# Optimization experiments

Hardware: AMD Instinct MI355X
Metric: run time of the kernel (lower is better)

## Reference

```python
import jax, jax.numpy as jnp
import numpy as np

INF = 1e10  # stand-in for +inf boundary of soft-DTW DP (safe under exp(-INF/gamma)=0)
HUBER_DELTA = 1.0
SDTW_ALPHA = 0.1
SDTW_GAMMA = 0.1


def _softmin3(a, b, c, gamma):
    # soft-min_gamma(a,b,c) = -gamma * logsumexp(-a/g, -b/g, -c/g)
    s = jnp.stack([a, b, c], axis=0) * (-1.0 / gamma)
    return -gamma * jax.nn.logsumexp(s, axis=0)


def _soft_dtw(x, y, gamma):
    # x, y: (B, L, C). Returns per-batch soft-DTW value R[L-1, L-1], shape (B,).
    B, L, C = x.shape
    # pairwise squared-euclidean distances (B, L, L) without (B,L,L,C) blowup
    x2 = jnp.sum(x * x, axis=-1)  # (B, L)
    y2 = jnp.sum(y * y, axis=-1)  # (B, L)
    D = x2[:, :, None] + y2[:, None, :] - 2.0 * jnp.einsum('blc,bmc->blm', x, y)

    i = jnp.arange(L)

    # Diagonals are stored as (B, L+1) arrays indexed by p = i + 1, so that the
    # virtual cell R[-1,-1] = 0 lives at p = 0 of diagonal k = -2.
    def step(carry, k):
        r2, r1 = carry  # diagonals k-2 and k-1
        j = k - i
        valid = (j >= 0) & (j < L)
        jc = jnp.clip(j, 0, L - 1)
        d = jnp.take_along_axis(D, jc[None, :, None], axis=2)[:, :, 0]  # (B, L) = D[:, i, k-i]
        a = r2[:, :-1]  # R[i-1, j-1]
        b = r1[:, :-1]  # R[i-1, j]
        c = r1[:, 1:]   # R[i, j-1]
        rk_vals = jnp.where(valid[None, :], d + _softmin3(a, b, c, gamma), INF)
        rk = jnp.concatenate([jnp.full((B, 1), INF, D.dtype), rk_vals], axis=1)
        return (r1, rk), None

    r2 = jnp.full((B, L + 1), INF, D.dtype).at[:, 0].set(0.0)  # diag k=-2: R[-1,-1]=0
    r1 = jnp.full((B, L + 1), INF, D.dtype)                    # diag k=-1: all inf
    (_, rlast), _ = jax.lax.scan(step, (r2, r1), jnp.arange(2 * L - 1))
    return rlast[:, L]  # R[L-1, L-1] per batch


def _huber_mean(x_hat, x, delta):
    d = x_hat - x
    ad = jnp.abs(d)
    loss = jnp.where(ad <= delta, 0.5 * d * d, delta * (ad - 0.5 * delta))
    return jnp.mean(loss)


def setup_inputs() -> dict:
    key = jax.random.key(0)
    k1, k2, k3 = jax.random.split(key, 3)
    B, L, C = 64, 512, 16
    x = jax.random.normal(k1, (B, L, C), dtype=jnp.float32)
    x_hat = jax.random.normal(k2, (B, L, C), dtype=jnp.float32)
    commitment_loss = jax.random.uniform(k3, (), dtype=jnp.float32)
    return {"x": x, "x_hat": x_hat, "commitment_loss": commitment_loss}


def reference(x, x_hat, commitment_loss):
    huber = _huber_mean(x_hat, x, HUBER_DELTA)
    sdtw = jnp.mean(_soft_dtw(x, x_hat, SDTW_GAMMA)) * SDTW_ALPHA
    total = huber + sdtw + commitment_loss
    # stacked [total, huber, sdtw, commitment] (torch module returns a dict of these scalars)
    return jnp.stack([total, huber, sdtw, commitment_loss])
```

## Files before the change

kernel.cpp:

```cpp
#include <hip/hip_runtime.h>
#include <math.h>


#define INFV 1.0e10f
static constexpr float kC1 = 14.4269504088896f;
static constexpr float kC2 = 0.0693147180559945f;

__device__ __forceinline__ int diag_off(int k) {
  if (k <= 512) return (k * (k + 1)) >> 1;
  int u = k - 512;
  return 131328 + 511 * u - ((u * (u - 1)) >> 1);
}
__device__ __forceinline__ int diag_i0(int k) { return k < 512 ? 0 : k - 511; }

__device__ __forceinline__ float huber1(float d) {
  float ad = fabsf(d);
  return ad <= 1.0f ? 0.5f * d * d : ad - 0.5f;
}

__global__ __launch_bounds__(256) void huber_kernel(const float* __restrict__ x,
                                                    const float* __restrict__ xh,
                                                    float* __restrict__ part) {
  int t = threadIdx.x;
  int gid = blockIdx.x * 256 + t;
  float s = 0.f;
  for (int i = gid; i < 131072; i += 65536) {
    float4 a = ((const float4*)x)[i];
    float4 b = ((const float4*)xh)[i];
    s += huber1(b.x - a.x) + huber1(b.y - a.y) + huber1(b.z - a.z) + huber1(b.w - a.w);
  }
  for (int o = 32; o > 0; o >>= 1) s += __shfl_down(s, o, 64);
  __shared__ float ws4[4];
  if ((t & 63) == 0) ws4[t >> 6] = s;
  __syncthreads();
  if (t == 0) part[blockIdx.x] = ws4[0] + ws4[1] + ws4[2] + ws4[3];
}

__global__ __launch_bounds__(256) void gemm_diag_kernel(const float* __restrict__ x,
                                                        const float* __restrict__ xh,
                                                        float* __restrict__ Dp) {
  const int b = blockIdx.z;
  const int ti = blockIdx.x;
  const int tj = blockIdx.y;
  const int t = threadIdx.x;
  __shared__ float sm[64 * 67];
  float* xsT = sm;
  float* ysT = sm + 16 * 68;
  const float* xb = x + ((size_t)b * 8192) + ti * 1024;
  const float* yb = xh + ((size_t)b * 8192) + tj * 1024;
  {
    float4 xv = ((const float4*)xb)[t];
    float4 yv = ((const float4*)yb)[t];
    int r = t >> 2, c0 = (t & 3) << 2;
    xsT[(c0 + 0) * 68 + r] = xv.x;
    xsT[(c0 + 1) * 68 + r] = xv.y;
    xsT[(c0 + 2) * 68 + r] = xv.z;
    xsT[(c0 + 3) * 68 + r] = xv.w;
    ysT[(c0 + 0) * 68 + r] = yv.x;
    ysT[(c0 + 1) * 68 + r] = yv.y;
    ysT[(c0 + 2) * 68 + r] = yv.z;
    ysT[(c0 + 3) * 68 + r] = yv.w;
  }
  __syncthreads();
  const int tm = t & 15, tn = t >> 4;
  float acc[4][4] = {};
  float y2a[4] = {};
#pragma unroll
  for (int c = 0; c < 16; ++c) {
    float4 xv = *(const float4*)&xsT[c * 68 + tm * 4];
    float4 yv = *(const float4*)&ysT[c * 68 + tn * 4];
    float xr[4] = {xv.x, xv.y, xv.z, xv.w};
    float yr[4] = {yv.x, yv.y, yv.z, yv.w};
#pragma unroll
    for (int n = 0; n < 4; ++n) {
      y2a[n] = fmaf(yr[n], yr[n], y2a[n]);
#pragma unroll
      for (int m = 0; m < 4; ++m) acc[m][n] = fmaf(xr[m], yr[n], acc[m][n]);
    }
  }
  __syncthreads();
#pragma unroll
  for (int m = 0; m < 4; ++m)
#pragma unroll
    for (int n = 0; n < 4; ++n)
      sm[(tm * 4 + m) * 67 + (tn * 4 + n)] = acc[m][n] - 0.5f * y2a[n];
  __syncthreads();
  const int lane = t & 63, wv = t >> 6;
  float* outb = Dp + (size_t)b * 262144;
  const int kbase = ti * 64 + tj * 64;
  for (int s = wv; s < 127; s += 4) {
    int ilo = s > 63 ? s - 63 : 0;
    int ihi = s < 63 ? s : 63;
    if (lane >= ilo && lane <= ihi) {
      float v = sm[lane * 67 + (s - lane)];
      int k = kbase + s;
      outb[diag_off(k) - diag_i0(k) + (ti * 64 + lane)] = v;
    }
  }
}

#define DTW_STEP(PD, W, R1, R2)                                             \
  do {                                                                      \
    int j = k - tid;                                                        \
    bool valid = (j >= 0) && (j < 512);                                     \
    float av = R2[tid];                                                     \
    float bv = R1[tid];                                                     \
    float dotv = PD;                                                        \
    if (k + 3 <= 1022) PD = Db[diag_off(k + 3) - diag_i0(k + 3) + tid];     \
    float mv = fminf(fminf(av, bv), vprev);                                 \
    float ssum = exp2f((mv - av) * kC1) + exp2f((mv - bv) * kC1) +          \
                 exp2f((mv - vprev) * kC1);                                 \
    float sm3 = fmaf(-kC2, log2f(ssum), mv);                                \
    float dd = fmaf(-2.0f, dotv, x2);                                       \
    float val = valid ? (dd + sm3) : INFV;                                  \
    W[tid + 1] = val;                                                       \
    vprev = val;                                                            \
    __syncthreads();                                                        \
    ++k;                                                                    \
  } while (0)

__global__ __launch_bounds__(512) void dtw_kernel(const float* __restrict__ x,
                                                  const float* __restrict__ Dp,
                                                  float* __restrict__ outv) {
  const int b = blockIdx.x;
  const int tid = threadIdx.x;
  __shared__ float rA[516], rB[516], rC[516];
  const float* xr = x + (size_t)b * 8192 + tid * 16;
  float x2 = 0.f;
#pragma unroll
  for (int c = 0; c < 16; c += 4) {
    float4 v = *(const float4*)(xr + c);
    x2 += v.x * v.x + v.y * v.y + v.z * v.z + v.w * v.w;
  }
  rA[tid] = INFV;
  rB[tid] = INFV;
  rC[tid] = INFV;
  if (tid == 0) { rA[512] = INFV; rB[512] = INFV; rC[512] = INFV; }
  const float* Db = Dp + (size_t)b * 262144;
  float p0 = Db[tid];
  float p1 = Db[1 + tid];
  float p2 = Db[3 + tid];
  float d00 = fmaf(-2.0f, p0, x2);
  float vprev = (tid == 0) ? d00 : INFV;
  if (tid == 0) rC[1] = d00;
  p0 = Db[diag_off(3) + tid];
  int k = 1;
  __syncthreads();
#pragma unroll 1
  for (int it = 0; it < 340; ++it) {
    DTW_STEP(p1, rA, rC, rB);
    DTW_STEP(p2, rB, rA, rC);
    DTW_STEP(p0, rC, rB, rA);
  }
  DTW_STEP(p1, rA, rC, rB);
  DTW_STEP(p2, rB, rA, rC);
  if (tid == 511) outv[b] = vprev;
}

__device__ __forceinline__ float dot16(const float4& a, const float4& b2,
                                       const float4& c, const float4& d,
                                       const float4* yp) {
  float4 q0 = yp[0], q1 = yp[1], q2 = yp[2], q3 = yp[3];
  float s = a.x * q0.x;
  s = fmaf(a.y, q0.y, s); s = fmaf(a.z, q0.z, s); s = fmaf(a.w, q0.w, s);
  s = fmaf(b2.x, q1.x, s); s = fmaf(b2.y, q1.y, s); s = fmaf(b2.z, q1.z, s); s = fmaf(b2.w, q1.w, s);
  s = fmaf(c.x, q2.x, s); s = fmaf(c.y, q2.y, s); s = fmaf(c.z, q2.z, s); s = fmaf(c.w, q2.w, s);
  s = fmaf(d.x, q3.x, s); s = fmaf(d.y, q3.y, s); s = fmaf(d.z, q3.z, s); s = fmaf(d.w, q3.w, s);
  return s;
}

#define DTW_FSTEP(W, R1, R2)                                                \
  do {                                                                      \
    int j = k - tid;                                                        \
    bool valid = (j >= 0) && (j < 512);                                     \
    int jc = valid ? j : 0;                                                 \
    float av = R2[tid];                                                     \
    float bv = R1[tid];                                                     \
    float dotv = dot16(xa, xb4, xc4, xd4, (const float4*)&ysl[jc * 20]);    \
    float mv = fminf(fminf(av, bv), vprev);                                 \
    float ssum = exp2f((mv - av) * kC1) + exp2f((mv - bv) * kC1) +          \
                 exp2f((mv - vprev) * kC1);                                 \
    float sm3 = fmaf(-kC2, log2f(ssum), mv);                                \
    float dd = fmaf(-2.0f, dotv, x2 + y2s[jc]);                             \
    float val = valid ? (dd + sm3) : INFV;                                  \
    W[tid + 1] = val;                                                       \
    vprev = val;                                                            \
    __syncthreads();                                                        \
    ++k;                                                                    \
  } while (0)

__global__ __launch_bounds__(512) void dtw_fused_kernel(const float* __restrict__ x,
                                                        const float* __restrict__ xh,
                                                        float* __restrict__ outv) {
  const int b = blockIdx.x;
  const int tid = threadIdx.x;
  __shared__ float ysl[512 * 20];
  __shared__ float y2s[512];
  __shared__ float rA[516], rB[516], rC[516];
  const float* xr = x + (size_t)b * 8192 + tid * 16;
  const float* yr = xh + (size_t)b * 8192 + tid * 16;
  float4 xa = *(const float4*)(xr + 0);
  float4 xb4 = *(const float4*)(xr + 4);
  float4 xc4 = *(const float4*)(xr + 8);
  float4 xd4 = *(const float4*)(xr + 12);
  float x2 = xa.x * xa.x + xa.y * xa.y + xa.z * xa.z + xa.w * xa.w +
             xb4.x * xb4.x + xb4.y * xb4.y + xb4.z * xb4.z + xb4.w * xb4.w +
             xc4.x * xc4.x + xc4.y * xc4.y + xc4.z * xc4.z + xc4.w * xc4.w +
             xd4.x * xd4.x + xd4.y * xd4.y + xd4.z * xd4.z + xd4.w * xd4.w;
  {
    float4 q0 = *(const float4*)(yr + 0);
    float4 q1 = *(const float4*)(yr + 4);
    float4 q2 = *(const float4*)(yr + 8);
    float4 q3 = *(const float4*)(yr + 12);
    *(float4*)&ysl[tid * 20 + 0] = q0;
    *(float4*)&ysl[tid * 20 + 4] = q1;
    *(float4*)&ysl[tid * 20 + 8] = q2;
    *(float4*)&ysl[tid * 20 + 12] = q3;
    y2s[tid] = q0.x * q0.x + q0.y * q0.y + q0.z * q0.z + q0.w * q0.w +
               q1.x * q1.x + q1.y * q1.y + q1.z * q1.z + q1.w * q1.w +
               q2.x * q2.x + q2.y * q2.y + q2.z * q2.z + q2.w * q2.w +
               q3.x * q3.x + q3.y * q3.y + q3.z * q3.z + q3.w * q3.w;
  }
  rA[tid] = INFV;
  rB[tid] = INFV;
  rC[tid] = INFV;
  if (tid == 0) { rA[512] = INFV; rB[512] = INFV; rC[512] = INFV; }
  __syncthreads();
  float dot00 = dot16(xa, xb4, xc4, xd4, (const float4*)&ysl[0]);
  float d00 = fmaf(-2.0f, dot00, x2 + y2s[0]);
  float vprev = (tid == 0) ? d00 : INFV;
  if (tid == 0) rC[1] = d00;
  int k = 1;
  __syncthreads();
#pragma unroll 1
  for (int it = 0; it < 340; ++it) {
    DTW_FSTEP(rA, rC, rB);
    DTW_FSTEP(rB, rA, rC);
    DTW_FSTEP(rC, rB, rA);
  }
  DTW_FSTEP(rA, rC, rB);
  DTW_FSTEP(rB, rA, rC);
  if (tid == 511) outv[b] = vprev;
}

__global__ __launch_bounds__(256) void finalize_kernel(const float* __restrict__ part,
                                                       const float* __restrict__ dtwv,
                                                       const float* __restrict__ commit,
                                                       float* __restrict__ out) {
  int t = threadIdx.x;
  float h = part[t];
  float dv = (t < 64) ? dtwv[t] : 0.f;
  for (int o = 32; o > 0; o >>= 1) {
    h += __shfl_down(h, o, 64);
    dv += __shfl_down(dv, o, 64);
  }
  __shared__ float sh[4], sd[4];
  if ((t & 63) == 0) { sh[t >> 6] = h; sd[t >> 6] = dv; }
  __syncthreads();
  if (t == 0) {
    float hs = sh[0] + sh[1] + sh[2] + sh[3];
    float ds = sd[0] + sd[1] + sd[2] + sd[3];
    float hm = hs * (1.0f / 524288.0f);
    float smv = ds * (0.1f / 64.0f);
    float cm = commit[0];
    out[0] = hm + smv + cm;
    out[1] = hm;
    out[2] = smv;
    out[3] = cm;
  }
}

extern "C" void kernel_launch(void* const* d_in, const int* in_sizes, int n_in,
                              void* d_out, int out_size, void* d_ws, size_t ws_size,
                              hipStream_t stream) {
  (void)in_sizes; (void)n_in; (void)out_size;
  const float* x = (const float*)d_in[0];
  const float* xh = (const float*)d_in[1];
  const float* commit = (const float*)d_in[2];
  float* out = (float*)d_out;
  float* ws = (float*)d_ws;
  float* part = ws;
  float* dtwv = ws + 256;
  float* Dp = ws + 512;
  const size_t need = 2048 + (size_t)64 * 262144 * 4;

  huber_kernel<<<256, 256, 0, stream>>>(x, xh, part);
  if (ws_size >= need) {
    gemm_diag_kernel<<<dim3(8, 8, 64), 256, 0, stream>>>(x, xh, Dp);
    dtw_kernel<<<64, 512, 0, stream>>>(x, Dp, dtwv);
  } else {
    dtw_fused_kernel<<<64, 512, 0, stream>>>(x, xh, dtwv);
  }
  finalize_kernel<<<1, 256, 0, stream>>>(part, dtwv, commit, out);
}
```

Baseline: 383.9 us.

## Replace per-diagonal block barriers with wavefront-pipelined soft-DTW using shuffles and flags

Replaces the original DTW kernel, which called __syncthreads after every anti-diagonal step. In the new kernel each 64-lane wavefront owns 64 rows and passes the neighbouring cell by __shfl_up within the wave. Between waves, the last lane's values go through a shared-memory ring buffer guarded by spin-wait flags, checked once every 10 steps. Softmin now sorts its three inputs with min/med3/max, which saves one exp2 per cell. D loads are prefetched 10 diagonals ahead. Spin-waiting on volatile shared flags adds pipeline fill latency and depends on memory ordering being correct.

```diff
diff --git a/kernel.cpp b/kernel.cpp
--- a/kernel.cpp
+++ b/kernel.cpp
@@ -99,61 +99,84 @@
   }
 }
 
-#define DTW_STEP(PD, W, R1, R2)                                             \
+#define PSTEP(PN)                                                           \
   do {                                                                      \
-    int j = k - tid;                                                        \
-    bool valid = (j >= 0) && (j < 512);                                     \
-    float av = R2[tid];                                                     \
-    float bv = R1[tid];                                                     \
-    float dotv = PD;                                                        \
-    if (k + 3 <= 1022) PD = Db[diag_off(k + 3) - diag_i0(k + 3) + tid];     \
-    float mv = fminf(fminf(av, bv), vprev);                                 \
-    float ssum = exp2f((mv - av) * kC1) + exp2f((mv - bv) * kC1) +          \
-                 exp2f((mv - vprev) * kC1);                                 \
+    float bval = __shfl_up(vprev, 1);                                       \
+    float rv = ringPrev[min(kk + 63, 574)];                                 \
+    if (lane == 0) bval = (w == 0) ? INFV : rv;                             \
+    float mv = fminf(fminf(aval, bval), vprev);                             \
+    float md = __builtin_amdgcn_fmed3f(aval, bval, vprev);                  \
+    float mx = fmaxf(fmaxf(aval, bval), vprev);                             \
+    float ssum = 1.0f + exp2f((mv - md) * kC1) + exp2f((mv - mx) * kC1);    \
     float sm3 = fmaf(-kC2, log2f(ssum), mv);                                \
+    float dotv = PN;                                                        \
+    {                                                                       \
+      int kc = k0 + min(kk + 10, 574);                                      \
+      PN = DbL[diag_off(kc) - diag_i0(kc)];                                 \
+    }                                                                       \
     float dd = fmaf(-2.0f, dotv, x2);                                       \
-    float val = valid ? (dd + sm3) : INFV;                                  \
-    W[tid + 1] = val;                                                       \
+    float val = ((unsigned)(kk - lane) <= 511u) ? (dd + sm3) : INFV;        \
+    if (lane == 63) ringOwn[kk] = val;                                      \
+    aval = bval;                                                            \
     vprev = val;                                                            \
-    __syncthreads();                                                        \
-    ++k;                                                                    \
+    ++kk;                                                                   \
   } while (0)
 
-__global__ __launch_bounds__(512) void dtw_kernel(const float* __restrict__ x,
-                                                  const float* __restrict__ Dp,
-                                                  float* __restrict__ outv) {
+__global__ __launch_bounds__(512) void dtw_pipe_kernel(const float* __restrict__ x,
+                                                       const float* __restrict__ Dp,
+                                                       float* __restrict__ outv) {
   const int b = blockIdx.x;
   const int tid = threadIdx.x;
-  __shared__ float rA[516], rB[516], rC[516];
-  const float* xr = x + (size_t)b * 8192 + tid * 16;
+  const int w = tid >> 6;
+  const int lane = tid & 63;
+  __shared__ float ring[8][576];
+  __shared__ int flags[8];
+  if (tid < 8) flags[tid] = 0;
+  __syncthreads();
+  volatile int* vflags = flags;
+
+  const int i = (w << 6) | lane;
+  const float* xr = x + (size_t)b * 8192 + i * 16;
   float x2 = 0.f;
 #pragma unroll
   for (int c = 0; c < 16; c += 4) {
     float4 v = *(const float4*)(xr + c);
     x2 += v.x * v.x + v.y * v.y + v.z * v.z + v.w * v.w;
   }
-  rA[tid] = INFV;
-  rB[tid] = INFV;
-  rC[tid] = INFV;
-  if (tid == 0) { rA[512] = INFV; rB[512] = INFV; rC[512] = INFV; }
-  const float* Db = Dp + (size_t)b * 262144;
-  float p0 = Db[tid];
-  float p1 = Db[1 + tid];
-  float p2 = Db[3 + tid];
-  float d00 = fmaf(-2.0f, p0, x2);
-  float vprev = (tid == 0) ? d00 : INFV;
-  if (tid == 0) rC[1] = d00;
-  p0 = Db[diag_off(3) + tid];
-  int k = 1;
-  __syncthreads();
+  const float* DbL = Dp + (size_t)b * 262144 + i;
+  const int k0 = w << 6;
+
+  float p[10];
+#pragma unroll
+  for (int n = 0; n < 10; ++n) {
+    int kg = k0 + n;
+    p[n] = DbL[diag_off(kg) - diag_i0(kg)];
+  }
+
+  float aval = (w == 0 && lane == 0) ? 0.0f : INFV;
+  float vprev = INFV;
+  float* ringOwn = ring[w];
+  const float* ringPrev = ring[(w == 0) ? 7 : (w - 1)];
+
+  int kk = 0;
 #pragma unroll 1
-  for (int it = 0; it < 340; ++it) {
-    DTW_STEP(p1, rA, rC, rB);
-    DTW_STEP(p2, rB, rA, rC);
-    DTW_STEP(p0, rC, rB, rA);
-  }
-  DTW_STEP(p1, rA, rC, rB);
-  DTW_STEP(p2, rB, rA, rC);
+  for (int ss = 0; ss < 58; ++ss) {
+    const int nsub = (ss == 57) ? 5 : 10;
+    if (w != 0) {
+      const int need = min(kk + nsub + 63, 575);
+      while (vflags[w - 1] < need) {
+      }
+      __threadfence_block();
+    }
+    if (nsub == 10) {
+      PSTEP(p[0]); PSTEP(p[1]); PSTEP(p[2]); PSTEP(p[3]); PSTEP(p[4]);
+      PSTEP(p[5]); PSTEP(p[6]); PSTEP(p[7]); PSTEP(p[8]); PSTEP(p[9]);
+    } else {
+      PSTEP(p[0]); PSTEP(p[1]); PSTEP(p[2]); PSTEP(p[3]); PSTEP(p[4]);
+    }
+    __threadfence_block();
+    if (lane == 63) vflags[w] = kk;
+  }
   if (tid == 511) outv[b] = vprev;
 }
 
@@ -164,7 +187,7 @@
   float s = a.x * q0.x;
   s = fmaf(a.y, q0.y, s); s = fmaf(a.z, q0.z, s); s = fmaf(a.w, q0.w, s);
   s = fmaf(b2.x, q1.x, s); s = fmaf(b2.y, q1.y, s); s = fmaf(b2.z, q1.z, s); s = fmaf(b2.w, q1.w, s);
-  s = fmaf(c.x, q2.x, s); s = fmaf(c.y, q2.y, s); s = fmaf(c.z, q2.z, s); s = fmaf(c.w, q2.w, s);
+  s = fmaf(c.x, q2.x, s); s = fmaf(c.y, q2.y, s); s = fmaf(c.w, q2.w, s); s = fmaf(c.z, q2.z, s);
   s = fmaf(d.x, q3.x, s); s = fmaf(d.y, q3.y, s); s = fmaf(d.z, q3.z, s); s = fmaf(d.w, q3.w, s);
   return s;
 }
@@ -287,7 +310,7 @@
   huber_kernel<<<256, 256, 0, stream>>>(x, xh, part);
   if (ws_size >= need) {
     gemm_diag_kernel<<<dim3(8, 8, 64), 256, 0, stream>>>(x, xh, Dp);
-    dtw_kernel<<<64, 512, 0, stream>>>(x, Dp, dtwv);
+    dtw_pipe_kernel<<<64, 512, 0, stream>>>(x, Dp, dtwv);
   } else {
     dtw_fused_kernel<<<64, 512, 0, stream>>>(x, xh, dtwv);
   }
```

After: 353.0 us. 8.1% less time.

## Run soft-DTW wavefront in one wave with 8 rows per lane via DPP

Applied to the files above, without the earlier changes.

Replaces the 512-thread, LDS-plus-barrier-per-diagonal DTW with a single 64-lane wavefront where each lane owns 8 consecutive rows in registers. Neighbour values move between lanes through DPP row shifts instead of shared memory and __syncthreads. The GEMM now writes a full pre-scaled (by 1/(gamma·ln2)) distance matrix transposed in row-major j order, replacing the diagonal-packed layout. The softmin is rewritten as min plus log2(1+2^(min-med)+2^(min-max)) with fmed3. This removes about 1000 block-wide barriers but serialises 8 cells per lane per step, and wave-level cross-row shifting must handle the row-of-16 boundaries correctly.

```diff
diff --git a/kernel.cpp b/kernel.cpp
--- a/kernel.cpp
+++ b/kernel.cpp
@@ -2,16 +2,9 @@
 #include <math.h>
 
 
-#define INFV 1.0e10f
+#define INFS 1.0e10f
 static constexpr float kC1 = 14.4269504088896f;
 static constexpr float kC2 = 0.0693147180559945f;
-
-__device__ __forceinline__ int diag_off(int k) {
-  if (k <= 512) return (k * (k + 1)) >> 1;
-  int u = k - 512;
-  return 131328 + 511 * u - ((u * (u - 1)) >> 1);
-}
-__device__ __forceinline__ int diag_i0(int k) { return k < 512 ? 0 : k - 511; }
 
 __device__ __forceinline__ float huber1(float d) {
   float ad = fabsf(d);
@@ -38,14 +31,13 @@
 
 __global__ __launch_bounds__(256) void gemm_diag_kernel(const float* __restrict__ x,
                                                         const float* __restrict__ xh,
-                                                        float* __restrict__ Dp) {
+                                                        float* __restrict__ E) {
   const int b = blockIdx.z;
   const int ti = blockIdx.x;
   const int tj = blockIdx.y;
   const int t = threadIdx.x;
-  __shared__ float sm[64 * 67];
-  float* xsT = sm;
-  float* ysT = sm + 16 * 68;
+  __shared__ float xsT[16 * 68];
+  __shared__ float ysT[16 * 68];
   const float* xb = x + ((size_t)b * 8192) + ti * 1024;
   const float* yb = xh + ((size_t)b * 8192) + tj * 1024;
   {
@@ -65,6 +57,7 @@
   const int tm = t & 15, tn = t >> 4;
   float acc[4][4] = {};
   float y2a[4] = {};
+  float x2a[4] = {};
 #pragma unroll
   for (int c = 0; c < 16; ++c) {
     float4 xv = *(const float4*)&xsT[c * 68 + tm * 4];
@@ -77,84 +70,94 @@
 #pragma unroll
       for (int m = 0; m < 4; ++m) acc[m][n] = fmaf(xr[m], yr[n], acc[m][n]);
     }
-  }
-  __syncthreads();
-#pragma unroll
-  for (int m = 0; m < 4; ++m)
-#pragma unroll
-    for (int n = 0; n < 4; ++n)
-      sm[(tm * 4 + m) * 67 + (tn * 4 + n)] = acc[m][n] - 0.5f * y2a[n];
-  __syncthreads();
-  const int lane = t & 63, wv = t >> 6;
-  float* outb = Dp + (size_t)b * 262144;
-  const int kbase = ti * 64 + tj * 64;
-  for (int s = wv; s < 127; s += 4) {
-    int ilo = s > 63 ? s - 63 : 0;
-    int ihi = s < 63 ? s : 63;
-    if (lane >= ilo && lane <= ihi) {
-      float v = sm[lane * 67 + (s - lane)];
-      int k = kbase + s;
-      outb[diag_off(k) - diag_i0(k) + (ti * 64 + lane)] = v;
-    }
-  }
-}
-
-#define DTW_STEP(PD, W, R1, R2)                                             \
-  do {                                                                      \
-    int j = k - tid;                                                        \
-    bool valid = (j >= 0) && (j < 512);                                     \
-    float av = R2[tid];                                                     \
-    float bv = R1[tid];                                                     \
-    float dotv = PD;                                                        \
-    if (k + 3 <= 1022) PD = Db[diag_off(k + 3) - diag_i0(k + 3) + tid];     \
-    float mv = fminf(fminf(av, bv), vprev);                                 \
-    float ssum = exp2f((mv - av) * kC1) + exp2f((mv - bv) * kC1) +          \
-                 exp2f((mv - vprev) * kC1);                                 \
-    float sm3 = fmaf(-kC2, log2f(ssum), mv);                                \
-    float dd = fmaf(-2.0f, dotv, x2);                                       \
-    float val = valid ? (dd + sm3) : INFV;                                  \
-    W[tid + 1] = val;                                                       \
-    vprev = val;                                                            \
-    __syncthreads();                                                        \
-    ++k;                                                                    \
+#pragma unroll
+    for (int m = 0; m < 4; ++m) x2a[m] = fmaf(xr[m], xr[m], x2a[m]);
+  }
+  float* Eb = E + (size_t)b * 262144;
+  const int icol = ti * 64 + tm * 4;
+#pragma unroll
+  for (int n = 0; n < 4; ++n) {
+    int jrow = tj * 64 + tn * 4 + n;
+    float4 o;
+    o.x = kC1 * fmaf(-2.0f, acc[0][n], x2a[0] + y2a[n]);
+    o.y = kC1 * fmaf(-2.0f, acc[1][n], x2a[1] + y2a[n]);
+    o.z = kC1 * fmaf(-2.0f, acc[2][n], x2a[2] + y2a[n]);
+    o.w = kC1 * fmaf(-2.0f, acc[3][n], x2a[3] + y2a[n]);
+    *(float4*)&Eb[(size_t)jrow * 512 + icol] = o;
+  }
+}
+
+__device__ __forceinline__ float cellv(float a, float b, float c, float d) {
+  float mv = fminf(fminf(a, b), c);
+  float md = __builtin_amdgcn_fmed3f(a, b, c);
+  float mx = fmaxf(fmaxf(a, b), c);
+  float e1 = exp2f(mv - md);
+  float e2 = exp2f(mv - mx);
+  float lg = log2f(1.0f + e1 + e2);
+  return mv + d - lg;
+}
+
+#define STEP(P)                                                                        \
+  do {                                                                                 \
+    float r7old = R7;                                                                  \
+    int vi7 = __float_as_int(r7old);                                                   \
+    float bs = __int_as_float(__builtin_amdgcn_update_dpp(0, vi7, 0x111, 0xF, 0xF, true)); \
+    float bbr = __int_as_float(__builtin_amdgcn_update_dpp(0, vi7, 0x142, 0xF, 0xF, true)); \
+    float tb = fixl ? bbr : bs;                                                        \
+    tb = isl0 ? INFS : tb;                                                             \
+    float old0 = R0; R0 = cellv(taPrev, tb, R0, eL##P.x);                              \
+    float old1 = R1; R1 = cellv(old0, R0, R1, eL##P.y);                                \
+    float old2 = R2; R2 = cellv(old1, R1, R2, eL##P.z);                                \
+    float old3 = R3; R3 = cellv(old2, R2, R3, eL##P.w);                                \
+    float old4 = R4; R4 = cellv(old3, R3, R4, eH##P.x);                                \
+    float old5 = R5; R5 = cellv(old4, R4, R5, eH##P.y);                                \
+    float old6 = R6; R6 = cellv(old5, R5, R6, eH##P.z);                                \
+    R7 = cellv(old6, R6, R7, eH##P.w);                                                 \
+    taPrev = tb;                                                                       \
+    int jn = s + 4 - t;                                                                \
+    jn = jn < 0 ? 0 : (jn > 511 ? 511 : jn);                                           \
+    const float4* ep = (const float4*)(baseL + ((size_t)jn << 9));                     \
+    eL##P = ep[0];                                                                     \
+    eH##P = ep[1];                                                                     \
+    ++s;                                                                               \
   } while (0)
 
-__global__ __launch_bounds__(512) void dtw_kernel(const float* __restrict__ x,
-                                                  const float* __restrict__ Dp,
-                                                  float* __restrict__ outv) {
+__global__ __launch_bounds__(64) void dtw_r8_kernel(const float* __restrict__ E,
+                                                    float* __restrict__ outv) {
   const int b = blockIdx.x;
-  const int tid = threadIdx.x;
-  __shared__ float rA[516], rB[516], rC[516];
-  const float* xr = x + (size_t)b * 8192 + tid * 16;
-  float x2 = 0.f;
-#pragma unroll
-  for (int c = 0; c < 16; c += 4) {
-    float4 v = *(const float4*)(xr + c);
-    x2 += v.x * v.x + v.y * v.y + v.z * v.z + v.w * v.w;
-  }
-  rA[tid] = INFV;
-  rB[tid] = INFV;
-  rC[tid] = INFV;
-  if (tid == 0) { rA[512] = INFV; rB[512] = INFV; rC[512] = INFV; }
-  const float* Db = Dp + (size_t)b * 262144;
-  float p0 = Db[tid];
-  float p1 = Db[1 + tid];
-  float p2 = Db[3 + tid];
-  float d00 = fmaf(-2.0f, p0, x2);
-  float vprev = (tid == 0) ? d00 : INFV;
-  if (tid == 0) rC[1] = d00;
-  p0 = Db[diag_off(3) + tid];
-  int k = 1;
-  __syncthreads();
+  const int t = threadIdx.x;
+  const bool isl0 = (t == 0);
+  const bool fixl = ((t & 15) == 0) && (t != 0);
+  const float* baseL = E + (size_t)b * 262144 + t * 8;
+
+  float4 eL0, eH0, eL1, eH1, eL2, eH2, eL3, eH3;
+  {
+    int j0 = 0 - t; j0 = j0 < 0 ? 0 : j0;
+    int j1 = 1 - t; j1 = j1 < 0 ? 0 : j1;
+    int j2 = 2 - t; j2 = j2 < 0 ? 0 : j2;
+    int j3 = 3 - t; j3 = j3 < 0 ? 0 : j3;
+    const float4* p0 = (const float4*)(baseL + ((size_t)j0 << 9));
+    const float4* p1 = (const float4*)(baseL + ((size_t)j1 << 9));
+    const float4* p2 = (const float4*)(baseL + ((size_t)j2 << 9));
+    const float4* p3 = (const float4*)(baseL + ((size_t)j3 << 9));
+    eL0 = p0[0]; eH0 = p0[1];
+    eL1 = p1[0]; eH1 = p1[1];
+    eL2 = p2[0]; eH2 = p2[1];
+    eL3 = p3[0]; eH3 = p3[1];
+  }
+
+  float R0 = INFS, R1 = INFS, R2 = INFS, R3 = INFS;
+  float R4 = INFS, R5 = INFS, R6 = INFS, R7 = INFS;
+  float taPrev = isl0 ? 0.0f : INFS;
+  int s = 0;
+
 #pragma unroll 1
-  for (int it = 0; it < 340; ++it) {
-    DTW_STEP(p1, rA, rC, rB);
-    DTW_STEP(p2, rB, rA, rC);
-    DTW_STEP(p0, rC, rB, rA);
-  }
-  DTW_STEP(p1, rA, rC, rB);
-  DTW_STEP(p2, rB, rA, rC);
-  if (tid == 511) outv[b] = vprev;
+  for (int it = 0; it < 143; ++it) {
+    STEP(0); STEP(1); STEP(2); STEP(3);
+  }
+  STEP(0); STEP(1); STEP(2);
+
+  if (t == 63) outv[b] = R7 * kC2;
 }
 
 __device__ __forceinline__ float dot16(const float4& a, const float4& b2,
@@ -169,20 +172,20 @@
   return s;
 }
 
-#define DTW_FSTEP(W, R1, R2)                                                \
+#define DTW_FSTEP(W, R1v, R2v)                                              \
   do {                                                                      \
     int j = k - tid;                                                        \
     bool valid = (j >= 0) && (j < 512);                                     \
     int jc = valid ? j : 0;                                                 \
-    float av = R2[tid];                                                     \
-    float bv = R1[tid];                                                     \
+    float av = R2v[tid];                                                    \
+    float bv = R1v[tid];                                                    \
     float dotv = dot16(xa, xb4, xc4, xd4, (const float4*)&ysl[jc * 20]);    \
     float mv = fminf(fminf(av, bv), vprev);                                 \
     float ssum = exp2f((mv - av) * kC1) + exp2f((mv - bv) * kC1) +          \
                  exp2f((mv - vprev) * kC1);                                 \
     float sm3 = fmaf(-kC2, log2f(ssum), mv);                                \
     float dd = fmaf(-2.0f, dotv, x2 + y2s[jc]);                             \
-    float val = valid ? (dd + sm3) : INFV;                                  \
+    float val = valid ? (dd + sm3) : INFS;                                  \
     W[tid + 1] = val;                                                       \
     vprev = val;                                                            \
     __syncthreads();                                                        \
@@ -221,14 +224,14 @@
                q2.x * q2.x + q2.y * q2.y + q2.z * q2.z + q2.w * q2.w +
                q3.x * q3.x + q3.y * q3.y + q3.z * q3.z + q3.w * q3.w;
   }
-  rA[tid] = INFV;
-  rB[tid] = INFV;
-  rC[tid] = INFV;
-  if (tid == 0) { rA[512] = INFV; rB[512] = INFV; rC[512] = INFV; }
+  rA[tid] = INFS;
+  rB[tid] = INFS;
+  rC[tid] = INFS;
+  if (tid == 0) { rA[512] = INFS; rB[512] = INFS; rC[512] = INFS; }
   __syncthreads();
   float dot00 = dot16(xa, xb4, xc4, xd4, (const float4*)&ysl[0]);
   float d00 = fmaf(-2.0f, dot00, x2 + y2s[0]);
-  float vprev = (tid == 0) ? d00 : INFV;
+  float vprev = (tid == 0) ? d00 : INFS;
   if (tid == 0) rC[1] = d00;
   int k = 1;
   __syncthreads();
@@ -281,13 +284,13 @@
   float* ws = (float*)d_ws;
   float* part = ws;
   float* dtwv = ws + 256;
-  float* Dp = ws + 512;
+  float* E = ws + 512;
   const size_t need = 2048 + (size_t)64 * 262144 * 4;
 
   huber_kernel<<<256, 256, 0, stream>>>(x, xh, part);
   if (ws_size >= need) {
-    gemm_diag_kernel<<<dim3(8, 8, 64), 256, 0, stream>>>(x, xh, Dp);
-    dtw_kernel<<<64, 512, 0, stream>>>(x, Dp, dtwv);
+    gemm_diag_kernel<<<dim3(8, 8, 64), 256, 0, stream>>>(x, xh, E);
+    dtw_r8_kernel<<<64, 64, 0, stream>>>(E, dtwv);
   } else {
     dtw_fused_kernel<<<64, 512, 0, stream>>>(x, xh, dtwv);
   }
```

After: 412.2 us. 7.4% more time.
